# Kernel tuning notes

Measured on AMD Instinct MI355X. Metric: run time of the kernel, lower is better.

Reference implementation:

```python
import jax, jax.numpy as jnp
import numpy as np

_SIGMA = 1.5
_K1 = 0.01
_K2 = 0.03
WINDOW_SIZE = 11
VALUE_RANGE = 1.0


def gaussian_window(size: int, sigma: float) -> jnp.ndarray:
    # 1D gaussian, normalized; 2D window is the outer product (sums to 1)
    coords = jnp.arange(size, dtype=jnp.float32) - (size - 1) / 2.0
    g = jnp.exp(-(coords ** 2) / (2.0 * sigma ** 2))
    g = g / g.sum()
    return jnp.outer(g, g)  # (k, k)


def depthwise_conv(img, win2d):
    # img: (N, C, H, W), win2d: (k, k); depthwise valid conv, groups=C
    C = img.shape[1]
    kern = jnp.broadcast_to(win2d[:, :, None, None], win2d.shape + (1, C))  # HWIO
    return jax.lax.conv_general_dilated(
        img, kern, window_strides=(1, 1), padding='VALID',
        dimension_numbers=('NCHW', 'HWIO', 'NCHW'), feature_group_count=C)


def setup_inputs() -> dict:
    key = jax.random.key(0)
    k1, k2 = jax.random.split(key)
    x = jax.random.uniform(k1, (16, 3, 512, 512), dtype=jnp.float32)
    y = jax.random.uniform(k2, (16, 3, 512, 512), dtype=jnp.float32)
    window = gaussian_window(WINDOW_SIZE, _SIGMA)
    return {'x': x, 'y': y, 'window': window}


def reference(x, y, window):
    mu_x = depthwise_conv(x, window)
    mu_y = depthwise_conv(y, window)
    mu_x_sq = mu_x ** 2
    mu_y_sq = mu_y ** 2
    mu_xy = mu_x * mu_y
    sigma_x_sq = depthwise_conv(x * x, window) - mu_x_sq
    sigma_y_sq = depthwise_conv(y * y, window) - mu_y_sq
    sigma_xy = depthwise_conv(x * y, window) - mu_xy
    c1 = (_K1 * VALUE_RANGE) ** 2
    c2 = (_K2 * VALUE_RANGE) ** 2
    cs_map = (2.0 * sigma_xy + c2) / (sigma_x_sq + sigma_y_sq + c2)
    ssim_map = (2.0 * mu_xy + c1) / (mu_x_sq + mu_y_sq + c1) * cs_map
    # mean over spatial dims -> (N, C), mean over channels -> (N,), reduction='mean' -> scalar
    return ssim_map.mean(axis=(-1, -2)).mean(axis=-1).mean()
```

## Files before the change

### kernel.cpp

```cpp
#include <hip/hip_runtime.h>
#include <math.h>

#define KS    11
#define H     512
#define W     512
#define OH    502
#define OW    502
#define NPLANES 48
#define TOTAL_OUT (NPLANES * OH * OW)

#define TH      4
#define IROWS   (TH + KS - 1)
#define NSIG    4
#define LVW     523
#define NTHREADS 512
#define CHUNK   32
#define ITERS   (CHUNK / TH)
#define NCHUNKS 16

__global__ void zero_out_kernel(float* out) { out[0] = 0.0f; }

__global__ __launch_bounds__(NTHREADS, 3) void ssim_kernel(
    const float* __restrict__ x,
    const float* __restrict__ y,
    const float* __restrict__ win,
    float* __restrict__ out)
{
    __shared__ float v[NSIG][TH][LVW];
    __shared__ float w1s[KS];
    __shared__ float wsum[NTHREADS / 64];

    const int t     = threadIdx.x;
    const int chunk = blockIdx.x;
    const int plane = blockIdx.y;

    const int row_lo = chunk * CHUNK;
    const int row_hi = (row_lo + CHUNK < OH) ? (row_lo + CHUNK) : OH;

    const float* __restrict__ xp = x + (size_t)plane * (H * W);
    const float* __restrict__ yp = y + (size_t)plane * (H * W);

    if (t < KS) w1s[t] = sqrtf(win[t * KS + t]);
    __syncthreads();

    float w[KS];
#pragma unroll
    for (int k = 0; k < KS; k++) w[k] = w1s[k];

    const int r  = t & 3;
    const int c0 = (t >> 2) << 2;
    const float c1 = 1e-4f;
    const float c2 = 9e-4f;
    float acc = 0.f;

    for (int it = 0; it < ITERS; ++it) {
        const int gy0 = row_lo + it * TH;
        if (gy0 >= row_hi) break;

        float rxv[IROWS], ryv[IROWS];
#pragma unroll
        for (int j = 0; j < IROWS; j++) {
            int gy = gy0 + j; gy = (gy < H - 1) ? gy : (H - 1);
            rxv[j] = xp[gy * W + t];
            ryv[j] = yp[gy * W + t];
        }

        float a0[TH], a1[TH], a2[TH], a3[TH];
#pragma unroll
        for (int q = 0; q < TH; q++) { a0[q]=0.f; a1[q]=0.f; a2[q]=0.f; a3[q]=0.f; }

#pragma unroll
        for (int j = 0; j < IROWS; j++) {
            const float xv = rxv[j], yv = ryv[j];
            const float pss = xv * xv + yv * yv;
            const float pxy = xv * yv;
#pragma unroll
            for (int q = 0; q < TH; q++) {
                if (j - q >= 0 && j - q < KS) {
                    const float wk = w[j - q];
                    a0[q] += wk * xv;
                    a1[q] += wk * yv;
                    a2[q] += wk * pss;
                    a3[q] += wk * pxy;
                }
            }
        }

        __syncthreads();
#pragma unroll
        for (int q = 0; q < TH; q++) {
            v[0][q][t] = a0[q];
            v[1][q][t] = a1[q];
            v[2][q][t] = a2[q];
            v[3][q][t] = a3[q];
        }
        __syncthreads();

        float mu[NSIG][TH];
#pragma unroll
        for (int s = 0; s < NSIG; s++) {
            const float* __restrict__ vrow = &v[s][r][c0];
            float vs[IROWS];
#pragma unroll
            for (int j = 0; j < IROWS; j++) vs[j] = vrow[j];
#pragma unroll
            for (int p = 0; p < TH; p++) {
                float m = 0.f;
#pragma unroll
                for (int k = 0; k < KS; k++) m += w[k] * vs[p + k];
                mu[s][p] = m;
            }
        }

        const int grow  = gy0 + r;
        const bool rowok = (grow < row_hi);
#pragma unroll
        for (int p = 0; p < TH; p++) {
            if (rowok && (c0 + p) < OW) {
                const float mux = mu[0][p], muy = mu[1][p];
                const float mxy = mux * muy;
                const float m2  = mux * mux + muy * muy;
                const float sss = mu[2][p] - m2;
                const float sxy = mu[3][p] - mxy;
                const float num = (2.f * sxy + c2) * (2.f * mxy + c1);
                const float den = (sss + c2) * (m2 + c1);
                acc += num * __builtin_amdgcn_rcpf(den);
            }
        }
    }

#pragma unroll
    for (int off = 32; off > 0; off >>= 1)
        acc += __shfl_down(acc, off, 64);

    if ((t & 63) == 0) wsum[t >> 6] = acc;
    __syncthreads();
    if (t == 0) {
        float s = 0.f;
#pragma unroll
        for (int i = 0; i < NTHREADS / 64; i++) s += wsum[i];
        atomicAdd(out, s * (1.0f / (float)TOTAL_OUT));
    }
}

extern "C" void kernel_launch(void* const* d_in, const int* in_sizes, int n_in,
                              void* d_out, int out_size, void* d_ws, size_t ws_size,
                              hipStream_t stream)
{
    const float* x   = (const float*)d_in[0];
    const float* y   = (const float*)d_in[1];
    const float* win = (const float*)d_in[2];
    float* out = (float*)d_out;

    zero_out_kernel<<<1, 1, 0, stream>>>(out);

    dim3 grid(NCHUNKS, NPLANES);
    ssim_kernel<<<grid, NTHREADS, 0, stream>>>(x, y, win, out);
}
```

Before: 165.4 us.

## Reuse sliding window of input rows in registers and prefetch next rows

Instead of reloading all 14 input rows per 4-row iteration, the kernel keeps a register ring of rows, shifts them and loads only the 4 new rows, issued before the horizontal pass so global loads overlap compute. Window weights are forced to be wave-uniform via readfirstlane so they can live in scalar registers. This cuts global/L2 load traffic roughly 3.5x but adds register moves and pressure under the 3-blocks occupancy bound.

```diff
diff --git a/kernel.cpp b/kernel.cpp
--- a/kernel.cpp
+++ b/kernel.cpp
@@ -15,10 +15,13 @@
 #define LVW     523
 #define NTHREADS 512
 #define CHUNK   32
-#define ITERS   (CHUNK / TH)
 #define NCHUNKS 16
 
 __global__ void zero_out_kernel(float* out) { out[0] = 0.0f; }
+
+__device__ __forceinline__ float uniform_f(float v) {
+    return __int_as_float(__builtin_amdgcn_readfirstlane(__float_as_int(v)));
+}
 
 __global__ __launch_bounds__(NTHREADS, 3) void ssim_kernel(
     const float* __restrict__ x,
@@ -36,6 +39,7 @@
 
     const int row_lo = chunk * CHUNK;
     const int row_hi = (row_lo + CHUNK < OH) ? (row_lo + CHUNK) : OH;
+    const int niter  = (row_hi - row_lo + TH - 1) / TH;
 
     const float* __restrict__ xp = x + (size_t)plane * (H * W);
     const float* __restrict__ yp = y + (size_t)plane * (H * W);
@@ -45,7 +49,7 @@
 
     float w[KS];
 #pragma unroll
-    for (int k = 0; k < KS; k++) w[k] = w1s[k];
+    for (int k = 0; k < KS; k++) w[k] = uniform_f(w1s[k]);
 
     const int r  = t & 3;
     const int c0 = (t >> 2) << 2;
@@ -53,17 +57,16 @@
     const float c2 = 9e-4f;
     float acc = 0.f;
 
-    for (int it = 0; it < ITERS; ++it) {
+    float rx[IROWS], ry[IROWS];
+#pragma unroll
+    for (int j = 0; j < IROWS; j++) {
+        int gy = row_lo + j; gy = (gy < H - 1) ? gy : (H - 1);
+        rx[j] = xp[gy * W + t];
+        ry[j] = yp[gy * W + t];
+    }
+
+    for (int it = 0; it < niter; ++it) {
         const int gy0 = row_lo + it * TH;
-        if (gy0 >= row_hi) break;
-
-        float rxv[IROWS], ryv[IROWS];
-#pragma unroll
-        for (int j = 0; j < IROWS; j++) {
-            int gy = gy0 + j; gy = (gy < H - 1) ? gy : (H - 1);
-            rxv[j] = xp[gy * W + t];
-            ryv[j] = yp[gy * W + t];
-        }
 
         float a0[TH], a1[TH], a2[TH], a3[TH];
 #pragma unroll
@@ -71,7 +74,7 @@
 
 #pragma unroll
         for (int j = 0; j < IROWS; j++) {
-            const float xv = rxv[j], yv = ryv[j];
+            const float xv = rx[j], yv = ry[j];
             const float pss = xv * xv + yv * yv;
             const float pxy = xv * yv;
 #pragma unroll
@@ -95,6 +98,21 @@
             v[3][q][t] = a3[q];
         }
         __syncthreads();
+
+        if (it + 1 < niter) {
+#pragma unroll
+            for (int j = 0; j < IROWS - TH; j++) {
+                rx[j] = rx[j + TH];
+                ry[j] = ry[j + TH];
+            }
+#pragma unroll
+            for (int j = 0; j < TH; j++) {
+                int gy = gy0 + IROWS + j;
+                gy = (gy < H - 1) ? gy : (H - 1);
+                rx[IROWS - TH + j] = xp[gy * W + t];
+                ry[IROWS - TH + j] = yp[gy * W + t];
+            }
+        }
 
         float mu[NSIG][TH];
 #pragma unroll
```

After: 153.1 us. -7.4%, faster.
